# Kernel optimization log

Hardware: AMD Instinct MI355X
Metric: run time of the kernel (lower is better)

## Reference

```python
import jax, jax.numpy as jnp
import numpy as np

BETA = 0.9
THRESHOLD = 1.0
DELTA_THRESH = 0.2  # spikegen.delta threshold in encoder
NUM_STEPS = 64


def heaviside(v):
    return (v > 0).astype(v.dtype)


def lif_layer(cur):
    """snntorch Leaky (reset_mechanism='subtract') over cur: [S, B, H].
    mem_new = beta*mem + cur - (mem_old > thr)*thr ; spk = (mem_new > thr)."""
    def step(mem, c):
        reset = heaviside(mem - THRESHOLD)
        mem_new = BETA * mem + c - reset * THRESHOLD
        spk = heaviside(mem_new - THRESHOLD)
        return mem_new, spk

    mem0 = jnp.zeros(cur.shape[1:], cur.dtype)
    _, spk_rec = jax.lax.scan(step, mem0, cur)
    return spk_rec  # [S, B, H]


def setup_inputs() -> dict:
    key = jax.random.key(0)
    ks = jax.random.split(key, 7)
    F_in, H1, H2, H3 = 512, 1024, 1024, 512
    x = jax.random.normal(ks[0], (256, 128, F_in), dtype=jnp.float32)
    def lin(k, out_d, in_d):
        kw, kb = jax.random.split(k)
        s = 1.0 / np.sqrt(in_d)
        W = jax.random.uniform(kw, (out_d, in_d), jnp.float32, -s, s)
        b = jax.random.uniform(kb, (out_d,), jnp.float32, -s, s)
        return W, b
    W0, b0 = lin(ks[1], H1, F_in)
    W1, b1 = lin(ks[2], H2, H1)
    W2, b2 = lin(ks[3], H3, H2)
    return {"x": x, "W0": W0, "b0": b0, "W1": W1, "b1": b1, "W2": W2, "b2": b2}


def reference(x, W0, b0, W1, b1, W2, b2):
    B, T, F_in = x.shape
    # SpikeEncoder 'delta': spikegen.delta diffs along dim 0 (batch here, faithful to torch call)
    prev = jnp.concatenate([x[:1], x[:-1]], axis=0)
    delta_spk = ((x - prev) >= DELTA_THRESH).astype(x.dtype)  # [B, T, F]
    # repeat over S then mean over T  ==  mean over T then broadcast over S
    spikes = jnp.broadcast_to(delta_spk.mean(axis=1), (NUM_STEPS, B, F_in))  # [S, B, F]
    for W, b in ((W0, b0), (W1, b1), (W2, b2)):
        cur = jnp.einsum('sbf,hf->sbh', spikes, W) + b  # batched fc across all steps
        spikes = lif_layer(cur)
    return spikes  # [S, B, H_last]
```

## Files before the change

### kernel.cpp

```cpp
#include <hip/hip_runtime.h>
#include <hip/hip_bf16.h>

#define S_STEPS 64

typedef __bf16 bf16x8 __attribute__((ext_vector_type(8)));
typedef float  f32x4  __attribute__((ext_vector_type(4)));
typedef int    i32x4  __attribute__((ext_vector_type(4)));

__device__ __forceinline__ void async16(const void* g, void* l) {
    __builtin_amdgcn_global_load_lds((const __attribute__((address_space(1))) void*)g,
                                     (__attribute__((address_space(3))) void*)l,
                                     16, 0, 0);
}

__global__ void snn_prep(const float4* __restrict__ xv, ushort4* __restrict__ r,
                         const float4* __restrict__ W0, ushort4* __restrict__ w0out,
                         const float4* __restrict__ W1, const float4* __restrict__ W2,
                         char4* __restrict__ w1out, char4* __restrict__ w2out) {
    constexpr int T = 128, F4 = 128;
    constexpr int NB_ENC = 512;
    constexpr int N0_4 = 1024 * 512 / 4;
    constexpr int NB_W0 = N0_4 / 256;
    constexpr int N1_4 = 1024 * 1024 / 4;
    constexpr int N2_4 = 512 * 1024 / 4;
    __shared__ int4 red[4][64];

    const int bid = blockIdx.x;
    if (bid < NB_ENC) {
        const int f4i = threadIdx.x & 63;
        const int tc  = threadIdx.x >> 6;
        const int b   = bid >> 1;
        const int f4  = (bid & 1) * 64 + f4i;
        int c0 = 0, c1 = 0, c2 = 0, c3 = 0;
        if (b > 0) {
            const float4* xb = xv + ((size_t)b * T + tc * 32) * F4 + f4;
            const float4* xp = xb - (size_t)T * F4;
            for (int t = 0; t < 32; ++t) {
                float4 a = xb[(size_t)t * F4];
                float4 p = xp[(size_t)t * F4];
                c0 += (__fsub_rn(a.x, p.x) >= 0.2f) ? 1 : 0;
                c1 += (__fsub_rn(a.y, p.y) >= 0.2f) ? 1 : 0;
                c2 += (__fsub_rn(a.z, p.z) >= 0.2f) ? 1 : 0;
                c3 += (__fsub_rn(a.w, p.w) >= 0.2f) ? 1 : 0;
            }
        }
        red[tc][f4i] = int4{c0, c1, c2, c3};
        __syncthreads();
        if (tc == 0) {
            int4 a = red[0][f4i], bb = red[1][f4i], cc = red[2][f4i], dd = red[3][f4i];
            int s0 = a.x + bb.x + cc.x + dd.x;
            int s1 = a.y + bb.y + cc.y + dd.y;
            int s2 = a.z + bb.z + cc.z + dd.z;
            int s3 = a.w + bb.w + cc.w + dd.w;
            ushort4 o;
            o.x = __hip_bfloat16_raw(__float2bfloat16((float)s0 * (1.0f / 128.0f))).x;
            o.y = __hip_bfloat16_raw(__float2bfloat16((float)s1 * (1.0f / 128.0f))).x;
            o.z = __hip_bfloat16_raw(__float2bfloat16((float)s2 * (1.0f / 128.0f))).x;
            o.w = __hip_bfloat16_raw(__float2bfloat16((float)s3 * (1.0f / 128.0f))).x;
            r[(size_t)b * F4 + f4] = o;
        }
    } else if (bid < NB_ENC + NB_W0) {
        int j = (bid - NB_ENC) * 256 + threadIdx.x;
        float4 w = W0[j];
        float wv[4] = {w.x, w.y, w.z, w.w};
        unsigned short hv[4], mv[4], lv[4];
        #pragma unroll
        for (int q = 0; q < 4; ++q) {
            __hip_bfloat16 hh = __float2bfloat16(wv[q]);
            float r1 = __fsub_rn(wv[q], __bfloat162float(hh));
            __hip_bfloat16 mm = __float2bfloat16(r1);
            float r2 = __fsub_rn(r1, __bfloat162float(mm));
            hv[q] = __hip_bfloat16_raw(hh).x;
            mv[q] = __hip_bfloat16_raw(mm).x;
            lv[q] = __hip_bfloat16_raw(__float2bfloat16(r2)).x;
        }
        w0out[j]             = ushort4{hv[0], hv[1], hv[2], hv[3]};
        w0out[j + N0_4]      = ushort4{mv[0], mv[1], mv[2], mv[3]};
        w0out[j + 2 * N0_4]  = ushort4{lv[0], lv[1], lv[2], lv[3]};
    } else {
        int i = (bid - NB_ENC - NB_W0) * 256 + threadIdx.x;
        const float4* W; char4* out; int n4; int j = i;
        if (j < N1_4) { W = W1; out = w1out; n4 = N1_4; }
        else { j -= N1_4; W = W2; out = w2out; n4 = N2_4; }
        float4 w = W[j];
        float wv[4] = {w.x, w.y, w.z, w.w};
        signed char d2v[4], d1v[4], d0v[4];
        #pragma unroll
        for (int q = 0; q < 4; ++q) {
            int e  = __float2int_rn(wv[q] * 134217728.0f);
            int d0 = (int)(signed char)(e & 0xff);
            int e1 = (e - d0) >> 8;
            int d1 = (int)(signed char)(e1 & 0xff);
            int d2 = (e1 - d1) >> 8;
            d0v[q] = (signed char)d0;
            d1v[q] = (signed char)d1;
            d2v[q] = (signed char)d2;
        }
        out[j]          = make_char4(d2v[0], d2v[1], d2v[2], d2v[3]);
        out[j + n4]     = make_char4(d1v[0], d1v[1], d1v[2], d1v[3]);
        out[j + 2 * n4] = make_char4(d0v[0], d0v[1], d0v[2], d0v[3]);
    }
}


__global__ __launch_bounds__(256, 2)
void snn_gemm_i8_w_lif(const signed char* __restrict__ A,
                       const signed char* __restrict__ Wq,
                       const float* __restrict__ bias,
                       signed char* __restrict__ Sout,
                       int M, int N, int K) {
    __shared__ __align__(16) char As[3 * 8192];
    __shared__ __align__(16) char Bs[3 * 16384];
    const int t    = threadIdx.x;
    const int wave = t >> 6;
    const int lane = t & 63;

    int m_idx, n_idx;
    {
        int gx = gridDim.x, gy = gridDim.y;
        int flat = blockIdx.y * gx + blockIdx.x;
        if ((gy & 7) == 0) {
            int x = flat & 7, local = flat >> 3, h = gy >> 3;
            m_idx = x * h + (local % h);
            n_idx = local / h;
        } else { m_idx = blockIdx.y; n_idx = blockIdx.x; }
    }
    const int m0 = m_idx * 128;
    const int n0 = n_idx * 256;
    const int wm = (wave >> 1) * 64;
    const int wn = (wave & 1) * 128;

    const int srow = lane >> 2;
    const int schk = ((lane & 3) + (lane >> 2) + (lane >> 4)) & 3;
    const int rho  = lane & 15;
    const int kap  = lane >> 4;
    const int foff = ((rho << 2) + ((kap - rho - (rho >> 2)) & 3)) * 16;

    const int KT = K >> 6;
    const int NT = 3 * KT;
    const size_t PK = (size_t)N * K;

    size_t aOff[2], bOff[4];
    #pragma unroll
    for (int q = 0; q < 2; ++q)
        aOff[q] = (size_t)(m0 + (wave * 2 + q) * 16 + srow) * K + schk * 16;
    #pragma unroll
    for (int q = 0; q < 4; ++q)
        bOff[q] = (size_t)(n0 + (wave * 4 + q) * 16 + srow) * K + schk * 16;

    i32x4 acc[4][8] = {};
    i32x4 afA[4], afB[4], bLo[4], bHi[4];

    auto stageT = [&](int p, int kt, int bsel) {
        const int kk = kt << 6;
        char* as = As + bsel * 8192;
        char* bs = Bs + bsel * 16384;
        #pragma unroll
        for (int q = 0; q < 2; ++q)
            async16(A + aOff[q] + kk, as + (wave * 2 + q) * 1024 + lane * 16);
        const signed char* Bw = Wq + (size_t)p * PK;
        #pragma unroll
        for (int q = 0; q < 4; ++q)
            async16(Bw + bOff[q] + kk, bs + (wave * 4 + q) * 1024 + lane * 16);
    };

    int sp = 0, skt = 2;
    int sbuf = 2, rbuf = 1;

    auto body = [&](int i, i32x4* afc, i32x4* afn) {
        if (i + 2 < NT) {
            stageT(sp, skt, sbuf);
            if (++skt == KT) { skt = 0; ++sp; }
            asm volatile("s_waitcnt vmcnt(6)" ::: "memory");
        } else {
            asm volatile("s_waitcnt vmcnt(0)" ::: "memory");
        }
        __builtin_amdgcn_s_barrier();
        const char* as = As + rbuf * 8192;
        const char* bs = Bs + rbuf * 16384;
        #pragma unroll
        for (int q = 0; q < 4; ++q)
            afn[q] = *(const i32x4*)&as[((wm >> 4) + q) * 1024 + foff];
        #pragma unroll
        for (int q = 0; q < 4; ++q)
            bLo[q] = *(const i32x4*)&bs[((wn >> 4) + q) * 1024 + foff];
        __builtin_amdgcn_sched_barrier(0);
        #pragma unroll
        for (int q = 0; q < 4; ++q)
            #pragma unroll
            for (int j = 0; j < 4; ++j)
                acc[q][4 + j] = __builtin_amdgcn_mfma_i32_16x16x64_i8(afc[q], bHi[j], acc[q][4 + j], 0, 0, 0);
        #pragma unroll
        for (int q = 0; q < 4; ++q)
            bHi[q] = *(const i32x4*)&bs[((wn >> 4) + 4 + q) * 1024 + foff];
        asm volatile("s_waitcnt lgkmcnt(0)" ::: "memory");
        __builtin_amdgcn_sched_barrier(0);
        if (((i + 1) & (KT - 1)) == 0) {
            #pragma unroll
            for (int q = 0; q < 4; ++q)
                #pragma unroll
                for (int j = 0; j < 8; ++j)
                    acc[q][j] = acc[q][j] * 256;
        }
        #pragma unroll
        for (int q = 0; q < 4; ++q)
            #pragma unroll
            for (int j = 0; j < 4; ++j)
                acc[q][j] = __builtin_amdgcn_mfma_i32_16x16x64_i8(afn[q], bLo[j], acc[q][j], 0, 0, 0);
        sbuf = (sbuf == 2) ? 0 : sbuf + 1;
        rbuf = (rbuf == 2) ? 0 : rbuf + 1;
    };

    stageT(0, 0, 0);
    stageT(0, 1, 1);
    asm volatile("s_waitcnt vmcnt(6)" ::: "memory");
    __builtin_amdgcn_s_barrier();
    {
        const char* as = As;
        const char* bs = Bs;
        #pragma unroll
        for (int q = 0; q < 4; ++q)
            afA[q] = *(const i32x4*)&as[((wm >> 4) + q) * 1024 + foff];
        #pragma unroll
        for (int q = 0; q < 4; ++q) {
            bLo[q] = *(const i32x4*)&bs[((wn >> 4) + q) * 1024 + foff];
            bHi[q] = *(const i32x4*)&bs[((wn >> 4) + 4 + q) * 1024 + foff];
        }
    }
    asm volatile("s_waitcnt lgkmcnt(0)" ::: "memory");
    __builtin_amdgcn_sched_barrier(0);
    #pragma unroll
    for (int q = 0; q < 4; ++q)
        #pragma unroll
        for (int j = 0; j < 4; ++j)
            acc[q][j] = __builtin_amdgcn_mfma_i32_16x16x64_i8(afA[q], bLo[j], acc[q][j], 0, 0, 0);

    for (int i = 0; i < NT - 2; i += 2) {
        body(i, afA, afB);
        body(i + 1, afB, afA);
    }
    body(NT - 2, afA, afB);
    #pragma unroll
    for (int q = 0; q < 4; ++q)
        #pragma unroll
        for (int j = 0; j < 4; ++j)
            acc[q][4 + j] = __builtin_amdgcn_mfma_i32_16x16x64_i8(afB[q], bHi[j], acc[q][4 + j], 0, 0, 0);

    const float SCALE = 7.450580596923828e-9f;
    float bb[8];
    #pragma unroll
    for (int j = 0; j < 8; ++j)
        bb[j] = bias[n0 + wn + j * 16 + (lane & 15)];
    #pragma unroll
    for (int i = 0; i < 4; ++i)
        #pragma unroll
        for (int j = 0; j < 8; ++j) {
            i32x4 v = acc[i][j];
            f32x4 c;
            #pragma unroll
            for (int r = 0; r < 4; ++r)
                c[r] = (float)v[r] * SCALE + bb[j];
            acc[i][j] = __builtin_bit_cast(i32x4, c);
        }
    float mj[8] = {0.f, 0.f, 0.f, 0.f, 0.f, 0.f, 0.f, 0.f};
    signed char* So = Sout + (size_t)(m0 + wm) * N;
    #pragma unroll
    for (int seg = 0; seg < 16; ++seg) {
        const int si = seg >> 2, sk = seg & 3;
        const int src = (lane & 15) | (((sk + 3) & 3) << 4);
        #pragma unroll
        for (int j = 0; j < 8; ++j) {
            float tin = __shfl(mj[j], src);
            if (seg > 0 && kap == sk) mj[j] = tin;
        }
        if (kap == sk) {
            #pragma unroll
            for (int j = 0; j < 8; ++j) {
                f32x4 c = __builtin_bit_cast(f32x4, acc[si][j]);
                const int ng = n0 + wn + j * 16 + (lane & 15);
                #pragma unroll
                for (int r = 0; r < 4; ++r) {
                    float rst = (mj[j] > 1.0f) ? 1.0f : 0.0f;
                    mj[j] = __fsub_rn(__fadd_rn(__fmul_rn(0.9f, mj[j]), c[r]), rst);
                    So[(size_t)(seg * 4 + r) * N + ng] = (mj[j] > 1.0f) ? (signed char)1 : (signed char)0;
                }
            }
        }
    }
}

__global__ __launch_bounds__(256, 2)
void snn_gemm_i8_n_lif(const signed char* __restrict__ A,
                       const signed char* __restrict__ Wq,
                       const float* __restrict__ bias,
                       float* __restrict__ Dout,
                       int M, int N, int K, int Bsz) {
    __shared__ __align__(16) char As[3 * 8192];
    __shared__ __align__(16) char Bs[3 * 8192];
    const int t    = threadIdx.x;
    const int wave = t >> 6;
    const int lane = t & 63;

    int m_idx, n_idx;
    {
        int gx = gridDim.x, gy = gridDim.y;
        int flat = blockIdx.y * gx + blockIdx.x;
        if ((gy & 7) == 0) {
            int x = flat & 7, local = flat >> 3, h = gy >> 3;
            m_idx = x * h + (local % h);
            n_idx = local / h;
        } else { m_idx = blockIdx.y; n_idx = blockIdx.x; }
    }
    const int m0 = m_idx * 128;
    const int n0 = n_idx * 128;
    const int wm = (wave & 1) * 64;
    const int wn = (wave >> 1) * 64;

    const int srow = lane >> 2;
    const int schk = ((lane & 3) + (lane >> 2) + (lane >> 4)) & 3;
    const int rho  = lane & 15;
    const int kap  = lane >> 4;
    const int foff = ((rho << 2) + ((kap - rho - (rho >> 2)) & 3)) * 16;

    const int KT = K >> 6;
    const int NT = 3 * KT;
    const size_t PK = (size_t)N * K;

    size_t aOff[2], bOff[2];
    #pragma unroll
    for (int q = 0; q < 2; ++q) {
        aOff[q] = (size_t)(m0 + (wave * 2 + q) * 16 + srow) * K + schk * 16;
        bOff[q] = (size_t)(n0 + (wave * 2 + q) * 16 + srow) * K + schk * 16;
    }

    i32x4 acc[4][4] = {};
    i32x4 afA[4], afB[4], bLo[2], bHi[2];

    auto stageT = [&](int p, int kt, int bsel) {
        const int kk = kt << 6;
        char* as = As + bsel * 8192;
        char* bs = Bs + bsel * 8192;
        const signed char* Bw = Wq + (size_t)p * PK;
        #pragma unroll
        for (int q = 0; q < 2; ++q) {
            async16(A  + aOff[q] + kk, as + (wave * 2 + q) * 1024 + lane * 16);
            async16(Bw + bOff[q] + kk, bs + (wave * 2 + q) * 1024 + lane * 16);
        }
    };

    int sp = 0, skt = 2;
    int sbuf = 2, rbuf = 1;

    auto body = [&](int i, i32x4* afc, i32x4* afn) {
        if (i + 2 < NT) {
            stageT(sp, skt, sbuf);
            if (++skt == KT) { skt = 0; ++sp; }
            asm volatile("s_waitcnt vmcnt(4)" ::: "memory");
        } else {
            asm volatile("s_waitcnt vmcnt(0)" ::: "memory");
        }
        __builtin_amdgcn_s_barrier();
        const char* as = As + rbuf * 8192;
        const char* bs = Bs + rbuf * 8192;
        #pragma unroll
        for (int q = 0; q < 4; ++q)
            afn[q] = *(const i32x4*)&as[((wm >> 4) + q) * 1024 + foff];
        #pragma unroll
        for (int q = 0; q < 2; ++q)
            bLo[q] = *(const i32x4*)&bs[((wn >> 4) + q) * 1024 + foff];
        __builtin_amdgcn_sched_barrier(0);
        #pragma unroll
        for (int q = 0; q < 4; ++q)
            #pragma unroll
            for (int j = 0; j < 2; ++j)
                acc[q][2 + j] = __builtin_amdgcn_mfma_i32_16x16x64_i8(afc[q], bHi[j], acc[q][2 + j], 0, 0, 0);
        #pragma unroll
        for (int q = 0; q < 2; ++q)
            bHi[q] = *(const i32x4*)&bs[((wn >> 4) + 2 + q) * 1024 + foff];
        asm volatile("s_waitcnt lgkmcnt(0)" ::: "memory");
        __builtin_amdgcn_sched_barrier(0);
        if (((i + 1) & (KT - 1)) == 0) {
            #pragma unroll
            for (int q = 0; q < 4; ++q)
                #pragma unroll
                for (int j = 0; j < 4; ++j)
                    acc[q][j] = acc[q][j] * 256;
        }
        #pragma unroll
        for (int q = 0; q < 4; ++q)
            #pragma unroll
            for (int j = 0; j < 2; ++j)
                acc[q][j] = __builtin_amdgcn_mfma_i32_16x16x64_i8(afn[q], bLo[j], acc[q][j], 0, 0, 0);
        sbuf = (sbuf == 2) ? 0 : sbuf + 1;
        rbuf = (rbuf == 2) ? 0 : rbuf + 1;
    };

    stageT(0, 0, 0);
    stageT(0, 1, 1);
    asm volatile("s_waitcnt vmcnt(4)" ::: "memory");
    __builtin_amdgcn_s_barrier();
    {
        const char* as = As;
        const char* bs = Bs;
        #pragma unroll
        for (int q = 0; q < 4; ++q)
            afA[q] = *(const i32x4*)&as[((wm >> 4) + q) * 1024 + foff];
        #pragma unroll
        for (int q = 0; q < 2; ++q) {
            bLo[q] = *(const i32x4*)&bs[((wn >> 4) + q) * 1024 + foff];
            bHi[q] = *(const i32x4*)&bs[((wn >> 4) + 2 + q) * 1024 + foff];
        }
    }
    asm volatile("s_waitcnt lgkmcnt(0)" ::: "memory");
    __builtin_amdgcn_sched_barrier(0);
    #pragma unroll
    for (int q = 0; q < 4; ++q)
        #pragma unroll
        for (int j = 0; j < 2; ++j)
            acc[q][j] = __builtin_amdgcn_mfma_i32_16x16x64_i8(afA[q], bLo[j], acc[q][j], 0, 0, 0);

    for (int i = 0; i < NT - 2; i += 2) {
        body(i, afA, afB);
        body(i + 1, afB, afA);
    }
    body(NT - 2, afA, afB);
    #pragma unroll
    for (int q = 0; q < 4; ++q)
        #pragma unroll
        for (int j = 0; j < 2; ++j)
            acc[q][2 + j] = __builtin_amdgcn_mfma_i32_16x16x64_i8(afB[q], bHi[j], acc[q][2 + j], 0, 0, 0);

    const float SCALE = 7.450580596923828e-9f;
    float bb[4];
    #pragma unroll
    for (int j = 0; j < 4; ++j)
        bb[j] = bias[n0 + wn + j * 16 + (lane & 15)];
    #pragma unroll
    for (int i = 0; i < 4; ++i)
        #pragma unroll
        for (int j = 0; j < 4; ++j) {
            i32x4 v = acc[i][j];
            f32x4 c;
            #pragma unroll
            for (int r = 0; r < 4; ++r)
                c[r] = (float)v[r] * SCALE + bb[j];
            acc[i][j] = __builtin_bit_cast(i32x4, c);
        }
    float mj[4] = {0.f, 0.f, 0.f, 0.f};
    const int b_idx = (m0 + wm) >> 6;
    #pragma unroll
    for (int seg = 0; seg < 16; ++seg) {
        const int si = seg >> 2, sk = seg & 3;
        const int src = (lane & 15) | (((sk + 3) & 3) << 4);
        #pragma unroll
        for (int j = 0; j < 4; ++j) {
            float tin = __shfl(mj[j], src);
            if (seg > 0 && kap == sk) mj[j] = tin;
        }
        if (kap == sk) {
            #pragma unroll
            for (int j = 0; j < 4; ++j) {
                f32x4 c = __builtin_bit_cast(f32x4, acc[si][j]);
                const int ng = n0 + wn + j * 16 + (lane & 15);
                #pragma unroll
                for (int r = 0; r < 4; ++r) {
                    float rst = (mj[j] > 1.0f) ? 1.0f : 0.0f;
                    mj[j] = __fsub_rn(__fadd_rn(__fmul_rn(0.9f, mj[j]), c[r]), rst);
                    Dout[((size_t)(seg * 4 + r) * Bsz + b_idx) * N + ng] = (mj[j] > 1.0f) ? 1.0f : 0.0f;
                }
            }
        }
    }
}

__global__ __launch_bounds__(256, 2)
void snn_gemm0_bf16p(const __hip_bfloat16* __restrict__ A,
                     const __hip_bfloat16* __restrict__ Wp,
                     float* __restrict__ Cpart) {
    constexpr int M = 256, N = 1024, K = 512;
    constexpr int KT = K / 32;
    __shared__ __align__(16) char As[3 * 8192];
    __shared__ __align__(16) char Bs[3 * 8192];
    const int t    = threadIdx.x;
    const int wave = t >> 6;
    const int lane = t & 63;

    const int part = blockIdx.z;
    const __hip_bfloat16* Bw = Wp + (size_t)part * N * K;
    float* C = Cpart + (size_t)part * M * N;
    const int m0 = blockIdx.y * 128;
    const int n0 = blockIdx.x * 128;
    const int wm = (wave & 1) * 64;
    const int wn = (wave >> 1) * 64;

    const int srow = lane >> 2;
    const int schk = ((lane & 3) + (lane >> 2) + (lane >> 4)) & 3;
    const int rho  = lane & 15;
    const int kap  = lane >> 4;
    const int foff = ((rho << 2) + ((kap - rho - (rho >> 2)) & 3)) * 16;

    size_t aOff[2], bOff[2];
    #pragma unroll
    for (int q = 0; q < 2; ++q) {
        aOff[q] = (size_t)(m0 + (wave * 2 + q) * 16 + srow) * K + schk * 8;
        bOff[q] = (size_t)(n0 + (wave * 2 + q) * 16 + srow) * K + schk * 8;
    }

    f32x4 acc[4][4] = {};
    bf16x8 afA[4], afB[4], bLo[2], bHi[2];

    auto stageT = [&](int kt, int bsel) {
        const int kk = kt << 5;
        char* as = As + bsel * 8192;
        char* bs = Bs + bsel * 8192;
        #pragma unroll
        for (int q = 0; q < 2; ++q) {
            async16(A  + aOff[q] + kk, as + (wave * 2 + q) * 1024 + lane * 16);
            async16(Bw + bOff[q] + kk, bs + (wave * 2 + q) * 1024 + lane * 16);
        }
    };

    int skt = 2;
    int sbuf = 2, rbuf = 1;

    auto body = [&](int i, bf16x8* afc, bf16x8* afn) {
        if (i + 2 < KT) {
            stageT(skt, sbuf);
            ++skt;
            asm volatile("s_waitcnt vmcnt(4)" ::: "memory");
        } else {
            asm volatile("s_waitcnt vmcnt(0)" ::: "memory");
        }
        __builtin_amdgcn_s_barrier();
        const char* as = As + rbuf * 8192;
        const char* bs = Bs + rbuf * 8192;
        #pragma unroll
        for (int q = 0; q < 4; ++q)
            afn[q] = *(const bf16x8*)&as[((wm >> 4) + q) * 1024 + foff];
        #pragma unroll
        for (int q = 0; q < 2; ++q)
            bLo[q] = *(const bf16x8*)&bs[((wn >> 4) + q) * 1024 + foff];
        __builtin_amdgcn_sched_barrier(0);
        #pragma unroll
        for (int q = 0; q < 4; ++q)
            #pragma unroll
            for (int j = 0; j < 2; ++j)
                acc[q][2 + j] = __builtin_amdgcn_mfma_f32_16x16x32_bf16(afc[q], bHi[j], acc[q][2 + j], 0, 0, 0);
        #pragma unroll
        for (int q = 0; q < 2; ++q)
            bHi[q] = *(const bf16x8*)&bs[((wn >> 4) + 2 + q) * 1024 + foff];
        asm volatile("s_waitcnt lgkmcnt(0)" ::: "memory");
        __builtin_amdgcn_sched_barrier(0);
        #pragma unroll
        for (int q = 0; q < 4; ++q)
            #pragma unroll
            for (int j = 0; j < 2; ++j)
                acc[q][j] = __builtin_amdgcn_mfma_f32_16x16x32_bf16(afn[q], bLo[j], acc[q][j], 0, 0, 0);
        sbuf = (sbuf == 2) ? 0 : sbuf + 1;
        rbuf = (rbuf == 2) ? 0 : rbuf + 1;
    };

    stageT(0, 0);
    stageT(1, 1);
    asm volatile("s_waitcnt vmcnt(4)" ::: "memory");
    __builtin_amdgcn_s_barrier();
    {
        const char* as = As;
        const char* bs = Bs;
        #pragma unroll
        for (int q = 0; q < 4; ++q)
            afA[q] = *(const bf16x8*)&as[((wm >> 4) + q) * 1024 + foff];
        #pragma unroll
        for (int q = 0; q < 2; ++q) {
            bLo[q] = *(const bf16x8*)&bs[((wn >> 4) + q) * 1024 + foff];
            bHi[q] = *(const bf16x8*)&bs[((wn >> 4) + 2 + q) * 1024 + foff];
        }
    }
    asm volatile("s_waitcnt lgkmcnt(0)" ::: "memory");
    __builtin_amdgcn_sched_barrier(0);
    #pragma unroll
    for (int q = 0; q < 4; ++q)
        #pragma unroll
        for (int j = 0; j < 2; ++j)
            acc[q][j] = __builtin_amdgcn_mfma_f32_16x16x32_bf16(afA[q], bLo[j], acc[q][j], 0, 0, 0);

    for (int i = 0; i < KT - 2; i += 2) {
        body(i, afA, afB);
        body(i + 1, afB, afA);
    }
    body(KT - 2, afA, afB);
    #pragma unroll
    for (int q = 0; q < 4; ++q)
        #pragma unroll
        for (int j = 0; j < 2; ++j)
            acc[q][2 + j] = __builtin_amdgcn_mfma_f32_16x16x32_bf16(afB[q], bHi[j], acc[q][2 + j], 0, 0, 0);

    #pragma unroll
    for (int i = 0; i < 4; ++i) {
        int mg = m0 + wm + i * 16 + (lane >> 4) * 4;
        #pragma unroll
        for (int j = 0; j < 4; ++j) {
            int ng = n0 + wn + j * 16 + (lane & 15);
            #pragma unroll
            for (int r = 0; r < 4; ++r)
                C[(size_t)(mg + r) * N + ng] = acc[i][j][r];
        }
    }
}

__global__ void snn_lif0_sum3(const float4* __restrict__ p, const float4* __restrict__ b4,
                              uchar4* __restrict__ spk) {
    constexpr int MN4 = 256 * 1024 / 4;
    constexpr int H4  = 256;
    int idx = blockIdx.x * blockDim.x + threadIdx.x;
    if (idx >= MN4) return;
    const int b  = idx >> 8;
    const int h4 = idx & 255;
    float4 h = p[idx], mm = p[idx + MN4], l = p[idx + 2 * MN4], bb = b4[h4];
    float4 c;
    c.x = __fadd_rn(__fadd_rn(__fadd_rn(h.x, mm.x), l.x), bb.x);
    c.y = __fadd_rn(__fadd_rn(__fadd_rn(h.y, mm.y), l.y), bb.y);
    c.z = __fadd_rn(__fadd_rn(__fadd_rn(h.z, mm.z), l.z), bb.z);
    c.w = __fadd_rn(__fadd_rn(__fadd_rn(h.w, mm.w), l.w), bb.w);
    uchar4* out = spk + (size_t)b * S_STEPS * H4 + h4;
    float m0 = 0.0f, m1 = 0.0f, m2 = 0.0f, m3 = 0.0f;
    for (int s = 0; s < S_STEPS; ++s) {
        float r0 = (m0 > 1.0f) ? 1.0f : 0.0f;
        float r1 = (m1 > 1.0f) ? 1.0f : 0.0f;
        float r2 = (m2 > 1.0f) ? 1.0f : 0.0f;
        float r3 = (m3 > 1.0f) ? 1.0f : 0.0f;
        m0 = __fsub_rn(__fadd_rn(__fmul_rn(0.9f, m0), c.x), r0);
        m1 = __fsub_rn(__fadd_rn(__fmul_rn(0.9f, m1), c.y), r1);
        m2 = __fsub_rn(__fadd_rn(__fmul_rn(0.9f, m2), c.z), r2);
        m3 = __fsub_rn(__fadd_rn(__fmul_rn(0.9f, m3), c.w), r3);
        uchar4 o;
        o.x = (m0 > 1.0f) ? 1 : 0;
        o.y = (m1 > 1.0f) ? 1 : 0;
        o.z = (m2 > 1.0f) ? 1 : 0;
        o.w = (m3 > 1.0f) ? 1 : 0;
        out[(size_t)s * H4] = o;
    }
}

extern "C" void kernel_launch(void* const* d_in, const int* in_sizes, int n_in,
                              void* d_out, int out_size, void* d_ws, size_t ws_size,
                              hipStream_t stream) {
    const float* x  = (const float*)d_in[0];
    const float* W0 = (const float*)d_in[1];
    const float* b0 = (const float*)d_in[2];
    const float* W1 = (const float*)d_in[3];
    const float* b1 = (const float*)d_in[4];
    const float* W2 = (const float*)d_in[5];
    const float* b2 = (const float*)d_in[6];

    const int B = 256, T = 128, F = 512, H1 = 1024, H2 = 1024, H3 = 512;
    const int SB = S_STEPS * B;

    char* w = (char*)d_ws;
    signed char*    spk0 = (signed char*)w;                 w += (size_t)SB * H1;
    signed char*    spk1 = (signed char*)w;                 w += (size_t)SB * H2;
    __hip_bfloat16* r_bf = (__hip_bfloat16*)w;              w += (size_t)B * F * 2;
    float*          cur0p = (float*)w;                      w += (size_t)3 * B * H1 * 4;
    __hip_bfloat16* W0s  = (__hip_bfloat16*)w;              w += (size_t)3 * H1 * F * 2;
    signed char*    W1q  = (signed char*)w;                 w += (size_t)3 * H2 * H1;
    signed char*    W2q  = (signed char*)w;                 w += (size_t)3 * H3 * H2;

    snn_prep<<<dim3(2560), dim3(256), 0, stream>>>(
        (const float4*)x, (ushort4*)r_bf,
        (const float4*)W0, (ushort4*)W0s,
        (const float4*)W1, (const float4*)W2,
        (char4*)W1q, (char4*)W2q);

    snn_gemm0_bf16p<<<dim3(H1 / 128, B / 128, 3), dim3(256), 0, stream>>>(
        r_bf, W0s, cur0p);

    snn_lif0_sum3<<<dim3(B * H1 / 4 / 256), dim3(256), 0, stream>>>(
        (const float4*)cur0p, (const float4*)b0, (uchar4*)spk0);

    snn_gemm_i8_w_lif<<<dim3(H2 / 256, SB / 128), dim3(256), 0, stream>>>(
        spk0, W1q, b1, spk1, SB, H2, H1);

    snn_gemm_i8_n_lif<<<dim3(H3 / 128, SB / 128), dim3(256), 0, stream>>>(
        spk1, W2q, b2, (float*)d_out, SB, H3, H2, B);
}
```

Before: 233.1 us.

## Rewrite layer-1 int8 GEMM as 256x256 tile, 8-wave, 8-phase pipelined kernel

Replaces the 128x256 tile, 4-wave triple-buffered int8 GEMM for the second layer with a 256x256 tile, 512-thread kernel that double-buffers 128-wide K tiles in 128 KB of LDS and splits each K step into four phases. Each phase interleaves async global-to-LDS staging of one quarter tile with LDS fragment loads and MFMA bursts run at raised priority. The larger tile is meant to raise arithmetic intensity and cut global traffic per output. The cost is heavy LDS use that limits how many blocks fit per CU, many barriers, and half as many blocks in the grid.

Measured after the change: 240.8 us. +3.3%, slower.

```diff
diff --git a/kernel.cpp b/kernel.cpp
--- a/kernel.cpp
+++ b/kernel.cpp
@@ -103,17 +103,18 @@
 }
 
 
-__global__ __launch_bounds__(256, 2)
-void snn_gemm_i8_w_lif(const signed char* __restrict__ A,
-                       const signed char* __restrict__ Wq,
-                       const float* __restrict__ bias,
-                       signed char* __restrict__ Sout,
-                       int M, int N, int K) {
-    __shared__ __align__(16) char As[3 * 8192];
-    __shared__ __align__(16) char Bs[3 * 16384];
+__global__ __launch_bounds__(512, 2)
+void snn_gemm_i8_8ph(const signed char* __restrict__ A,
+                     const signed char* __restrict__ Wq,
+                     const float* __restrict__ bias,
+                     signed char* __restrict__ Sout,
+                     int M, int N, int K) {
+    __shared__ __align__(16) char Lds[131072];
     const int t    = threadIdx.x;
     const int wave = t >> 6;
     const int lane = t & 63;
+    const int wr   = wave >> 2;
+    const int wc   = wave & 3;
 
     int m_idx, n_idx;
     {
@@ -125,10 +126,8 @@
             n_idx = local / h;
         } else { m_idx = blockIdx.y; n_idx = blockIdx.x; }
     }
-    const int m0 = m_idx * 128;
+    const int m0 = m_idx * 256;
     const int n0 = n_idx * 256;
-    const int wm = (wave >> 1) * 64;
-    const int wn = (wave & 1) * 128;
 
     const int srow = lane >> 2;
     const int schk = ((lane & 3) + (lane >> 2) + (lane >> 4)) & 3;
@@ -136,153 +135,140 @@
     const int kap  = lane >> 4;
     const int foff = ((rho << 2) + ((kap - rho - (rho >> 2)) & 3)) * 16;
 
-    const int KT = K >> 6;
+    const int KT = K >> 7;
     const int NT = 3 * KT;
     const size_t PK = (size_t)N * K;
 
-    size_t aOff[2], bOff[4];
-    #pragma unroll
-    for (int q = 0; q < 2; ++q)
-        aOff[q] = (size_t)(m0 + (wave * 2 + q) * 16 + srow) * K + schk * 16;
-    #pragma unroll
-    for (int q = 0; q < 4; ++q)
-        bOff[q] = (size_t)(n0 + (wave * 4 + q) * 16 + srow) * K + schk * 16;
-
-    i32x4 acc[4][8] = {};
-    i32x4 afA[4], afB[4], bLo[4], bHi[4];
-
-    auto stageT = [&](int p, int kt, int bsel) {
-        const int kk = kt << 6;
-        char* as = As + bsel * 8192;
-        char* bs = Bs + bsel * 16384;
-        #pragma unroll
-        for (int q = 0; q < 2; ++q)
-            async16(A + aOff[q] + kk, as + (wave * 2 + q) * 1024 + lane * 16);
-        const signed char* Bw = Wq + (size_t)p * PK;
-        #pragma unroll
-        for (int q = 0; q < 4; ++q)
-            async16(Bw + bOff[q] + kk, bs + (wave * 4 + q) * 1024 + lane * 16);
-    };
-
-    int sp = 0, skt = 2;
-    int sbuf = 2, rbuf = 1;
-
-    auto body = [&](int i, i32x4* afc, i32x4* afn) {
-        if (i + 2 < NT) {
-            stageT(sp, skt, sbuf);
-            if (++skt == KT) { skt = 0; ++sp; }
-            asm volatile("s_waitcnt vmcnt(6)" ::: "memory");
+    const size_t aB0 = (size_t)(m0 + (wave * 2) * 16 + srow) * K;
+    const size_t aB1 = aB0 + (size_t)16 * K;
+    const size_t bB0 = (size_t)(n0 + (wave * 2) * 16 + srow) * K;
+    const size_t bB1 = bB0 + (size_t)16 * K;
+    const int sOff = schk * 16;
+
+    i32x4 acc[8][4] = {};
+    i32x4 af[4], bf[4];
+
+    auto stageQ = [&](int p, int kt, int q, int bsel) {
+        const size_t ko = (size_t)(kt << 7) + ((q >> 1) << 6) + sOff;
+        char* d = Lds + (((bsel << 2) + q) << 14) + (wave << 11) + lane * 16;
+        if (!(q & 1)) {
+            async16(A + aB0 + ko, d);
+            async16(A + aB1 + ko, d + 1024);
         } else {
-            asm volatile("s_waitcnt vmcnt(0)" ::: "memory");
-        }
-        __builtin_amdgcn_s_barrier();
-        const char* as = As + rbuf * 8192;
-        const char* bs = Bs + rbuf * 16384;
-        #pragma unroll
-        for (int q = 0; q < 4; ++q)
-            afn[q] = *(const i32x4*)&as[((wm >> 4) + q) * 1024 + foff];
-        #pragma unroll
-        for (int q = 0; q < 4; ++q)
-            bLo[q] = *(const i32x4*)&bs[((wn >> 4) + q) * 1024 + foff];
-        __builtin_amdgcn_sched_barrier(0);
+            const signed char* Bw = Wq + (size_t)p * PK;
+            async16(Bw + bB0 + ko, d);
+            async16(Bw + bB1 + ko, d + 1024);
+        }
+    };
+    auto ldA = [&](int mh, int kh, int b) {
+        const char* base = Lds + (((b << 2) + (kh << 1)) << 14) + foff;
+        #pragma unroll
+        for (int q = 0; q < 4; ++q)
+            af[q] = *(const i32x4*)(base + (wr * 8 + mh * 4 + q) * 1024);
+    };
+    auto ldB = [&](int kh, int b) {
+        const char* base = Lds + (((b << 2) + (kh << 1) + 1) << 14) + foff;
+        #pragma unroll
+        for (int q = 0; q < 4; ++q)
+            bf[q] = *(const i32x4*)(base + (wc * 4 + q) * 1024);
+    };
+    auto mmac = [&](int mh) {
         #pragma unroll
         for (int q = 0; q < 4; ++q)
             #pragma unroll
             for (int j = 0; j < 4; ++j)
-                acc[q][4 + j] = __builtin_amdgcn_mfma_i32_16x16x64_i8(afc[q], bHi[j], acc[q][4 + j], 0, 0, 0);
-        #pragma unroll
-        for (int q = 0; q < 4; ++q)
-            bHi[q] = *(const i32x4*)&bs[((wn >> 4) + 4 + q) * 1024 + foff];
+                acc[mh * 4 + q][j] = __builtin_amdgcn_mfma_i32_16x16x64_i8(af[q], bf[j], acc[mh * 4 + q][j], 0, 0, 0);
+    };
+
+    stageQ(0, 0, 0, 0); stageQ(0, 0, 1, 0); stageQ(0, 0, 2, 0); stageQ(0, 0, 3, 0);
+    int sp = 0, skt = 1;
+    asm volatile("s_waitcnt vmcnt(4)" ::: "memory");
+    __builtin_amdgcn_s_barrier();
+
+    for (int i = 0; i < NT; ++i) {
+        const int b = i & 1;
+        const bool st = (i + 1 < NT);
+        if (st) stageQ(sp, skt, 0, b ^ 1);
+        ldA(0, 0, b); ldB(0, b);
+        __builtin_amdgcn_s_barrier();
         asm volatile("s_waitcnt lgkmcnt(0)" ::: "memory");
         __builtin_amdgcn_sched_barrier(0);
-        if (((i + 1) & (KT - 1)) == 0) {
-            #pragma unroll
-            for (int q = 0; q < 4; ++q)
+        if (i == KT || i == 2 * KT) {
+            #pragma unroll
+            for (int q = 0; q < 8; ++q)
                 #pragma unroll
-                for (int j = 0; j < 8; ++j)
+                for (int j = 0; j < 4; ++j)
                     acc[q][j] = acc[q][j] * 256;
         }
-        #pragma unroll
-        for (int q = 0; q < 4; ++q)
-            #pragma unroll
-            for (int j = 0; j < 4; ++j)
-                acc[q][j] = __builtin_amdgcn_mfma_i32_16x16x64_i8(afn[q], bLo[j], acc[q][j], 0, 0, 0);
-        sbuf = (sbuf == 2) ? 0 : sbuf + 1;
-        rbuf = (rbuf == 2) ? 0 : rbuf + 1;
-    };
-
-    stageT(0, 0, 0);
-    stageT(0, 1, 1);
-    asm volatile("s_waitcnt vmcnt(6)" ::: "memory");
-    __builtin_amdgcn_s_barrier();
-    {
-        const char* as = As;
-        const char* bs = Bs;
-        #pragma unroll
-        for (int q = 0; q < 4; ++q)
-            afA[q] = *(const i32x4*)&as[((wm >> 4) + q) * 1024 + foff];
-        #pragma unroll
-        for (int q = 0; q < 4; ++q) {
-            bLo[q] = *(const i32x4*)&bs[((wn >> 4) + q) * 1024 + foff];
-            bHi[q] = *(const i32x4*)&bs[((wn >> 4) + 4 + q) * 1024 + foff];
-        }
-    }
-    asm volatile("s_waitcnt lgkmcnt(0)" ::: "memory");
-    __builtin_amdgcn_sched_barrier(0);
-    #pragma unroll
-    for (int q = 0; q < 4; ++q)
-        #pragma unroll
-        for (int j = 0; j < 4; ++j)
-            acc[q][j] = __builtin_amdgcn_mfma_i32_16x16x64_i8(afA[q], bLo[j], acc[q][j], 0, 0, 0);
-
-    for (int i = 0; i < NT - 2; i += 2) {
-        body(i, afA, afB);
-        body(i + 1, afB, afA);
-    }
-    body(NT - 2, afA, afB);
-    #pragma unroll
-    for (int q = 0; q < 4; ++q)
-        #pragma unroll
-        for (int j = 0; j < 4; ++j)
-            acc[q][4 + j] = __builtin_amdgcn_mfma_i32_16x16x64_i8(afB[q], bHi[j], acc[q][4 + j], 0, 0, 0);
+        __builtin_amdgcn_s_setprio(1); mmac(0); __builtin_amdgcn_s_setprio(0);
+        __builtin_amdgcn_s_barrier();
+        if (st) stageQ(sp, skt, 1, b ^ 1);
+        ldA(1, 0, b);
+        __builtin_amdgcn_s_barrier();
+        asm volatile("s_waitcnt lgkmcnt(0)" ::: "memory");
+        __builtin_amdgcn_sched_barrier(0);
+        __builtin_amdgcn_s_setprio(1); mmac(1); __builtin_amdgcn_s_setprio(0);
+        if (st) asm volatile("s_waitcnt vmcnt(4)" ::: "memory");
+        else    asm volatile("s_waitcnt vmcnt(0)" ::: "memory");
+        __builtin_amdgcn_s_barrier();
+        if (st) stageQ(sp, skt, 2, b ^ 1);
+        ldA(0, 1, b); ldB(1, b);
+        __builtin_amdgcn_s_barrier();
+        asm volatile("s_waitcnt lgkmcnt(0)" ::: "memory");
+        __builtin_amdgcn_sched_barrier(0);
+        __builtin_amdgcn_s_setprio(1); mmac(0); __builtin_amdgcn_s_setprio(0);
+        __builtin_amdgcn_s_barrier();
+        if (st) stageQ(sp, skt, 3, b ^ 1);
+        ldA(1, 1, b);
+        __builtin_amdgcn_s_barrier();
+        asm volatile("s_waitcnt lgkmcnt(0)" ::: "memory");
+        __builtin_amdgcn_sched_barrier(0);
+        __builtin_amdgcn_s_setprio(1); mmac(1); __builtin_amdgcn_s_setprio(0);
+        if (st) asm volatile("s_waitcnt vmcnt(4)" ::: "memory");
+        __builtin_amdgcn_s_barrier();
+        if (st) { if (++skt == KT) { skt = 0; ++sp; } }
+    }
 
     const float SCALE = 7.450580596923828e-9f;
-    float bb[8];
-    #pragma unroll
-    for (int j = 0; j < 8; ++j)
-        bb[j] = bias[n0 + wn + j * 16 + (lane & 15)];
-    #pragma unroll
-    for (int i = 0; i < 4; ++i)
-        #pragma unroll
-        for (int j = 0; j < 8; ++j) {
-            i32x4 v = acc[i][j];
+    float bb[4];
+    #pragma unroll
+    for (int j = 0; j < 4; ++j)
+        bb[j] = bias[n0 + wc * 64 + j * 16 + rho];
+    #pragma unroll
+    for (int q = 0; q < 8; ++q)
+        #pragma unroll
+        for (int j = 0; j < 4; ++j) {
+            i32x4 v = acc[q][j];
             f32x4 c;
             #pragma unroll
             for (int r = 0; r < 4; ++r)
                 c[r] = (float)v[r] * SCALE + bb[j];
-            acc[i][j] = __builtin_bit_cast(i32x4, c);
-        }
-    float mj[8] = {0.f, 0.f, 0.f, 0.f, 0.f, 0.f, 0.f, 0.f};
-    signed char* So = Sout + (size_t)(m0 + wm) * N;
-    #pragma unroll
-    for (int seg = 0; seg < 16; ++seg) {
-        const int si = seg >> 2, sk = seg & 3;
-        const int src = (lane & 15) | (((sk + 3) & 3) << 4);
-        #pragma unroll
-        for (int j = 0; j < 8; ++j) {
-            float tin = __shfl(mj[j], src);
-            if (seg > 0 && kap == sk) mj[j] = tin;
-        }
-        if (kap == sk) {
-            #pragma unroll
-            for (int j = 0; j < 8; ++j) {
-                f32x4 c = __builtin_bit_cast(f32x4, acc[si][j]);
-                const int ng = n0 + wn + j * 16 + (lane & 15);
+            acc[q][j] = __builtin_bit_cast(i32x4, c);
+        }
+    #pragma unroll
+    for (int bi = 0; bi < 2; ++bi) {
+        float mj[4] = {0.f, 0.f, 0.f, 0.f};
+        signed char* So = Sout + (size_t)(m0 + wr * 128 + bi * 64) * N;
+        #pragma unroll
+        for (int seg = 0; seg < 16; ++seg) {
+            const int si = seg >> 2, sk = seg & 3;
+            const int src = rho | (((sk + 3) & 3) << 4);
+            #pragma unroll
+            for (int j = 0; j < 4; ++j) {
+                float tin = __shfl(mj[j], src);
+                if (seg > 0 && kap == sk) mj[j] = tin;
+            }
+            if (kap == sk) {
                 #pragma unroll
-                for (int r = 0; r < 4; ++r) {
-                    float rst = (mj[j] > 1.0f) ? 1.0f : 0.0f;
-                    mj[j] = __fsub_rn(__fadd_rn(__fmul_rn(0.9f, mj[j]), c[r]), rst);
-                    So[(size_t)(seg * 4 + r) * N + ng] = (mj[j] > 1.0f) ? (signed char)1 : (signed char)0;
+                for (int j = 0; j < 4; ++j) {
+                    f32x4 c = __builtin_bit_cast(f32x4, acc[bi * 4 + si][j]);
+                    const int ng = n0 + wc * 64 + j * 16 + rho;
+                    #pragma unroll
+                    for (int r = 0; r < 4; ++r) {
+                        float rst = (mj[j] > 1.0f) ? 1.0f : 0.0f;
+                        mj[j] = __fsub_rn(__fadd_rn(__fmul_rn(0.9f, mj[j]), c[r]), rst);
+                        So[(size_t)(seg * 4 + r) * N + ng] = (mj[j] > 1.0f) ? (signed char)1 : (signed char)0;
+                    }
                 }
             }
         }
@@ -677,7 +663,7 @@
     snn_lif0_sum3<<<dim3(B * H1 / 4 / 256), dim3(256), 0, stream>>>(
         (const float4*)cur0p, (const float4*)b0, (uchar4*)spk0);
 
-    snn_gemm_i8_w_lif<<<dim3(H2 / 256, SB / 128), dim3(256), 0, stream>>>(
+    snn_gemm_i8_8ph<<<dim3(H2 / 256, SB / 256), dim3(512), 0, stream>>>(
         spk0, W1q, b1, spk1, SB, H2, H1);
 
     snn_gemm_i8_n_lif<<<dim3(H3 / 128, SB / 128), dim3(256), 0, stream>>>(
```

## Transpose GEMM accumulators through LDS so each lane runs a full LIF scan

Applied to the files above, without the earlier changes.

Before the LIF recurrence, each wave writes its float accumulator tile into a swizzled LDS buffer that reuses the GEMM staging memory, then reads it back transposed so each lane owns one output column across all 64 time steps. The old path serialized the scan across 16 segments, using cross-lane shuffles and predicating off three quarters of the lanes at each step. Now all 64 lanes run the recurrence at once. Shared memory per block grows, which may limit occupancy at the 2-blocks launch bound, and a 64-float per-lane array raises register pressure.

Measured after the change: 214.6 us, median of 3. 1.09x faster.

```diff
diff --git a/kernel.cpp b/kernel.cpp
--- a/kernel.cpp
+++ b/kernel.cpp
@@ -109,8 +109,9 @@
                        const float* __restrict__ bias,
                        signed char* __restrict__ Sout,
                        int M, int N, int K) {
-    __shared__ __align__(16) char As[3 * 8192];
-    __shared__ __align__(16) char Bs[3 * 16384];
+    __shared__ __align__(16) char Smem[73728];
+    char* As = Smem;
+    char* Bs = Smem + 24576;
     const int t    = threadIdx.x;
     const int wave = t >> 6;
     const int lane = t & 63;
@@ -247,43 +248,54 @@
             acc[q][4 + j] = __builtin_amdgcn_mfma_i32_16x16x64_i8(afB[q], bHi[j], acc[q][4 + j], 0, 0, 0);
 
     const float SCALE = 7.450580596923828e-9f;
-    float bb[8];
-    #pragma unroll
-    for (int j = 0; j < 8; ++j)
-        bb[j] = bias[n0 + wn + j * 16 + (lane & 15)];
-    #pragma unroll
-    for (int i = 0; i < 4; ++i)
-        #pragma unroll
-        for (int j = 0; j < 8; ++j) {
-            i32x4 v = acc[i][j];
-            f32x4 c;
-            #pragma unroll
-            for (int r = 0; r < 4; ++r)
-                c[r] = (float)v[r] * SCALE + bb[j];
-            acc[i][j] = __builtin_bit_cast(i32x4, c);
-        }
-    float mj[8] = {0.f, 0.f, 0.f, 0.f, 0.f, 0.f, 0.f, 0.f};
-    signed char* So = Sout + (size_t)(m0 + wm) * N;
-    #pragma unroll
-    for (int seg = 0; seg < 16; ++seg) {
-        const int si = seg >> 2, sk = seg & 3;
-        const int src = (lane & 15) | (((sk + 3) & 3) << 4);
-        #pragma unroll
-        for (int j = 0; j < 8; ++j) {
-            float tin = __shfl(mj[j], src);
-            if (seg > 0 && kap == sk) mj[j] = tin;
-        }
-        if (kap == sk) {
+    {
+        float bb[8];
+        #pragma unroll
+        for (int j = 0; j < 8; ++j)
+            bb[j] = bias[n0 + wn + j * 16 + rho];
+        #pragma unroll
+        for (int si = 0; si < 4; ++si)
             #pragma unroll
             for (int j = 0; j < 8; ++j) {
-                f32x4 c = __builtin_bit_cast(f32x4, acc[si][j]);
-                const int ng = n0 + wn + j * 16 + (lane & 15);
+                i32x4 v = acc[si][j];
+                f32x4 c;
                 #pragma unroll
-                for (int r = 0; r < 4; ++r) {
-                    float rst = (mj[j] > 1.0f) ? 1.0f : 0.0f;
-                    mj[j] = __fsub_rn(__fadd_rn(__fmul_rn(0.9f, mj[j]), c[r]), rst);
-                    So[(size_t)(seg * 4 + r) * N + ng] = (mj[j] > 1.0f) ? (signed char)1 : (signed char)0;
+                for (int r = 0; r < 4; ++r)
+                    c[r] = (float)v[r] * SCALE + bb[j];
+                acc[si][j] = __builtin_bit_cast(i32x4, c);
+            }
+    }
+    __builtin_amdgcn_s_barrier();
+    {
+        char* wb = Smem + wave * 16384;
+        const int brow = m0 + wm;
+        #pragma unroll
+        for (int h = 0; h < 2; ++h) {
+            #pragma unroll
+            for (int si = 0; si < 4; ++si)
+                #pragma unroll
+                for (int jj = 0; jj < 4; ++jj) {
+                    const int c = jj * 16 + rho;
+                    const int k = si * 4 + kap;
+                    *(f32x4*)(wb + c * 256 + ((k ^ (c & 7)) << 4)) =
+                        __builtin_bit_cast(f32x4, acc[si][h * 4 + jj]);
                 }
+            asm volatile("s_waitcnt lgkmcnt(0)" ::: "memory");
+            float col[64];
+            #pragma unroll
+            for (int k = 0; k < 16; ++k) {
+                f32x4 v = *(const f32x4*)(wb + lane * 256 + ((k ^ (lane & 7)) << 4));
+                col[k * 4 + 0] = v[0]; col[k * 4 + 1] = v[1];
+                col[k * 4 + 2] = v[2]; col[k * 4 + 3] = v[3];
+            }
+            asm volatile("s_waitcnt lgkmcnt(0)" ::: "memory");
+            signed char* So = Sout + (size_t)brow * N + (n0 + wn + h * 64 + lane);
+            float m = 0.0f;
+            #pragma unroll
+            for (int s = 0; s < 64; ++s) {
+                float rst = (m > 1.0f) ? 1.0f : 0.0f;
+                m = __fsub_rn(__fadd_rn(__fmul_rn(0.9f, m), col[s]), rst);
+                So[(size_t)s * N] = (m > 1.0f) ? (signed char)1 : (signed char)0;
             }
         }
     }
@@ -295,8 +307,9 @@
                        const float* __restrict__ bias,
                        float* __restrict__ Dout,
                        int M, int N, int K, int Bsz) {
-    __shared__ __align__(16) char As[3 * 8192];
-    __shared__ __align__(16) char Bs[3 * 8192];
+    __shared__ __align__(16) char Smem[65536];
+    char* As = Smem;
+    char* Bs = Smem + 24576;
     const int t    = threadIdx.x;
     const int wave = t >> 6;
     const int lane = t & 63;
@@ -431,44 +444,52 @@
             acc[q][2 + j] = __builtin_amdgcn_mfma_i32_16x16x64_i8(afB[q], bHi[j], acc[q][2 + j], 0, 0, 0);
 
     const float SCALE = 7.450580596923828e-9f;
-    float bb[4];
-    #pragma unroll
-    for (int j = 0; j < 4; ++j)
-        bb[j] = bias[n0 + wn + j * 16 + (lane & 15)];
-    #pragma unroll
-    for (int i = 0; i < 4; ++i)
-        #pragma unroll
-        for (int j = 0; j < 4; ++j) {
-            i32x4 v = acc[i][j];
-            f32x4 c;
-            #pragma unroll
-            for (int r = 0; r < 4; ++r)
-                c[r] = (float)v[r] * SCALE + bb[j];
-            acc[i][j] = __builtin_bit_cast(i32x4, c);
-        }
-    float mj[4] = {0.f, 0.f, 0.f, 0.f};
-    const int b_idx = (m0 + wm) >> 6;
-    #pragma unroll
-    for (int seg = 0; seg < 16; ++seg) {
-        const int si = seg >> 2, sk = seg & 3;
-        const int src = (lane & 15) | (((sk + 3) & 3) << 4);
-        #pragma unroll
-        for (int j = 0; j < 4; ++j) {
-            float tin = __shfl(mj[j], src);
-            if (seg > 0 && kap == sk) mj[j] = tin;
-        }
-        if (kap == sk) {
+    {
+        float bb[4];
+        #pragma unroll
+        for (int j = 0; j < 4; ++j)
+            bb[j] = bias[n0 + wn + j * 16 + rho];
+        #pragma unroll
+        for (int si = 0; si < 4; ++si)
             #pragma unroll
             for (int j = 0; j < 4; ++j) {
-                f32x4 c = __builtin_bit_cast(f32x4, acc[si][j]);
-                const int ng = n0 + wn + j * 16 + (lane & 15);
+                i32x4 v = acc[si][j];
+                f32x4 c;
                 #pragma unroll
-                for (int r = 0; r < 4; ++r) {
-                    float rst = (mj[j] > 1.0f) ? 1.0f : 0.0f;
-                    mj[j] = __fsub_rn(__fadd_rn(__fmul_rn(0.9f, mj[j]), c[r]), rst);
-                    Dout[((size_t)(seg * 4 + r) * Bsz + b_idx) * N + ng] = (mj[j] > 1.0f) ? 1.0f : 0.0f;
-                }
+                for (int r = 0; r < 4; ++r)
+                    c[r] = (float)v[r] * SCALE + bb[j];
+                acc[si][j] = __builtin_bit_cast(i32x4, c);
             }
+    }
+    __builtin_amdgcn_s_barrier();
+    {
+        char* wb = Smem + wave * 16384;
+        const int b_idx = (m0 + wm) >> 6;
+        #pragma unroll
+        for (int si = 0; si < 4; ++si)
+            #pragma unroll
+            for (int j = 0; j < 4; ++j) {
+                const int c = j * 16 + rho;
+                const int k = si * 4 + kap;
+                *(f32x4*)(wb + c * 256 + ((k ^ (c & 7)) << 4)) =
+                    __builtin_bit_cast(f32x4, acc[si][j]);
+            }
+        asm volatile("s_waitcnt lgkmcnt(0)" ::: "memory");
+        float col[64];
+        #pragma unroll
+        for (int k = 0; k < 16; ++k) {
+            f32x4 v = *(const f32x4*)(wb + lane * 256 + ((k ^ (lane & 7)) << 4));
+            col[k * 4 + 0] = v[0]; col[k * 4 + 1] = v[1];
+            col[k * 4 + 2] = v[2]; col[k * 4 + 3] = v[3];
+        }
+        asm volatile("s_waitcnt lgkmcnt(0)" ::: "memory");
+        float* Do = Dout + (size_t)b_idx * N + (n0 + wn + lane);
+        float m = 0.0f;
+        #pragma unroll
+        for (int s = 0; s < 64; ++s) {
+            float rst = (m > 1.0f) ? 1.0f : 0.0f;
+            m = __fsub_rn(__fadd_rn(__fmul_rn(0.9f, m), col[s]), rst);
+            Do[(size_t)s * Bsz * N] = (m > 1.0f) ? 1.0f : 0.0f;
         }
     }
 }
```
